# Optimization experiments

Measured on AMD Instinct MI355X. Metric: run time of the kernel, lower is better.

Reference implementation:

```python
import jax, jax.numpy as jnp
import numpy as np

H = 12          # num_heads
LENS_T = 64     # template tokens
LENS_S = 256    # search tokens
KEEP = int(0.7 * LENS_S)  # 179 kept search tokens


def _ln(x, s, b):
    mu = jnp.mean(x, axis=-1, keepdims=True)
    var = jnp.mean(jnp.square(x - mu), axis=-1, keepdims=True)
    return (x - mu) / jnp.sqrt(var + 1e-5) * s + b


def setup_inputs() -> dict:
    key = jax.random.key(0)
    ks = jax.random.split(key, 8)
    B, C, Hh = 32, 768, 3072
    N = LENS_T + LENS_S
    w = lambda k, shape: jax.random.normal(k, shape, jnp.float32) * 0.02
    return {
        "x": jax.random.normal(ks[0], (B, N, C), jnp.float32),
        "global_index_t": jnp.tile(jnp.arange(LENS_T, dtype=jnp.int32), (B, 1)),
        "global_index_s": jnp.tile(jnp.arange(LENS_S, dtype=jnp.int32), (B, 1)),
        "norm1_s": jnp.ones((C,), jnp.float32), "norm1_b": jnp.zeros((C,), jnp.float32),
        "qkv_w": w(ks[1], (C, 3 * C)), "qkv_b": jnp.zeros((3 * C,), jnp.float32),
        "proj_w": w(ks[2], (C, C)), "proj_b": jnp.zeros((C,), jnp.float32),
        "norm2_s": jnp.ones((C,), jnp.float32), "norm2_b": jnp.zeros((C,), jnp.float32),
        "fc1_w": w(ks[3], (C, Hh)), "fc1_b": jnp.zeros((Hh,), jnp.float32),
        "fc2_w": w(ks[4], (Hh, C)), "fc2_b": jnp.zeros((C,), jnp.float32),
        "gcn_w": w(ks[5], (C, C)), "gcn_b": jnp.zeros((C,), jnp.float32),
        "norm3_s": jnp.ones((C,), jnp.float32), "norm3_b": jnp.zeros((C,), jnp.float32),
    }


def reference(x, global_index_t, global_index_s,
              norm1_s, norm1_b, qkv_w, qkv_b, proj_w, proj_b,
              norm2_s, norm2_b, fc1_w, fc1_b, fc2_w, fc2_b,
              gcn_w, gcn_b, norm3_s, norm3_b):
    B, N, C = x.shape
    hd = C // H
    scale = hd ** -0.5

    # --- attention (attn weights explicitly materialized) ---
    h = _ln(x, norm1_s, norm1_b)
    qkv = (h @ qkv_w + qkv_b).reshape(B, N, 3, H, hd).transpose(2, 0, 3, 1, 4)
    q, k, v = qkv[0], qkv[1], qkv[2]                      # [B,H,N,hd]
    attn = jax.nn.softmax(jnp.einsum('bhqd,bhkd->bhqk', q, k) * scale, axis=-1)
    xa = jnp.einsum('bhqk,bhkd->bhqd', attn, v).transpose(0, 2, 1, 3).reshape(B, N, C)
    xa = xa @ proj_w + proj_b
    x = x + xa

    # --- MLP ---
    x_res = x
    h2 = _ln(x, norm2_s, norm2_b)
    h2 = jax.nn.gelu(h2 @ fc1_w + fc1_b, approximate=False) @ fc2_w + fc2_b
    x = x_res + h2

    # --- GCN using template<->search attention as adjacency ---
    # adjacency = [[0, w_ts], [w_ts^T, 0]]; exploit block sparsity instead of
    # materializing the dense [B,N,N] matrix.
    w_ts = jnp.sum(attn[:, :, :LENS_T, LENS_T:], axis=1) / H   # [B,T,S]
    w_ts = jax.nn.softmax(w_ts, axis=2)
    support = x @ gcn_w + gcn_b
    out_t = jnp.einsum('bts,bsd->btd', w_ts, support[:, LENS_T:])   # top block
    out_s = jnp.einsum('bts,btd->bsd', w_ts, support[:, :LENS_T])   # bottom block
    x = jnp.concatenate([out_t, out_s], axis=1)
    x = x + _ln(x, norm3_s, norm3_b)

    # --- top-k token pruning on search tokens ---
    score_s = jnp.mean(attn[:, :, :LENS_T, LENS_T:], axis=(1, 2))   # [B,S]
    order = jnp.argsort(-score_s, axis=1)
    keep_indices = order[:, :KEEP]
    removed_index_s = order[:, KEEP:]
    gs_new = jnp.take_along_axis(global_index_s, keep_indices, axis=1)
    idx = jnp.concatenate([global_index_t.astype(jnp.int32), keep_indices + LENS_T], axis=1)
    x = jnp.take_along_axis(x, jnp.broadcast_to(idx[..., None], (B, idx.shape[1], C)), axis=1)
    return (x, global_index_t, gs_new, removed_index_s, attn)
```

## Files before the change

kernel.cpp:

```cpp
#include <hip/hip_runtime.h>
#include <math.h>

#define NKEEP 179
#define NREM  77
#define NOUT_ROWS 243

typedef __bf16 bf16x8 __attribute__((ext_vector_type(8)));
typedef float f32x4 __attribute__((ext_vector_type(4)));

__device__ __forceinline__ unsigned short f2bf(float f) {
  unsigned u = __builtin_bit_cast(unsigned, f);
  u = (u + 0x7FFFu + ((u >> 16) & 1u)) >> 16;
  return (unsigned short)u;
}

__device__ __forceinline__ void gload_lds16(const void* g, void* l) {
  __builtin_amdgcn_global_load_lds((const __attribute__((address_space(1))) void*)g,
                                   (__attribute__((address_space(3))) void*)l,
                                   16, 0, 0);
}

template<int RESID, int OUTMODE>
__global__ __launch_bounds__(256)
void ln_kernel(const float* __restrict__ in, const float* __restrict__ gs,
               const float* __restrict__ gb, void* __restrict__ outp,
               void* __restrict__ outp2) {
  int row = blockIdx.x;
  const float* p = in + (size_t)row * 768;
  int tid = threadIdx.x;
  float v0 = p[tid], v1 = p[tid + 256], v2 = p[tid + 512];
  __shared__ double rs[256], rq[256];
  double d0 = v0, d1 = v1, d2 = v2;
  rs[tid] = d0 + d1 + d2;
  rq[tid] = d0 * d0 + d1 * d1 + d2 * d2;
  __syncthreads();
  for (int st = 128; st > 0; st >>= 1) {
    if (tid < st) { rs[tid] += rs[tid + st]; rq[tid] += rq[tid + st]; }
    __syncthreads();
  }
  double mu  = rs[0] * (1.0 / 768.0);
  double var = rq[0] * (1.0 / 768.0) - mu * mu;
  float rstd = (float)rsqrt(var + 1e-5);
  float muf = (float)mu;
  float y0 = (v0 - muf) * rstd * gs[tid]       + gb[tid];
  float y1 = (v1 - muf) * rstd * gs[tid + 256] + gb[tid + 256];
  float y2 = (v2 - muf) * rstd * gs[tid + 512] + gb[tid + 512];
  if (RESID) { y0 += v0; y1 += v1; y2 += v2; }
  if (OUTMODE == 0 || OUTMODE == 2) {
    float* o = (float*)outp + (size_t)row * 768;
    o[tid] = y0; o[tid + 256] = y1; o[tid + 512] = y2;
  }
  if (OUTMODE == 1) {
    unsigned short* o = (unsigned short*)outp + (size_t)row * 768;
    o[tid] = f2bf(y0); o[tid + 256] = f2bf(y1); o[tid + 512] = f2bf(y2);
  }
  if (OUTMODE == 2) {
    unsigned short* o = (unsigned short*)outp2 + (size_t)row * 768;
    o[tid] = f2bf(y0); o[tid + 256] = f2bf(y1); o[tid + 512] = f2bf(y2);
  }
}

__global__ __launch_bounds__(256)
void wtrans_kernel(const float* __restrict__ W, unsigned short* __restrict__ Wt,
                   int K, int N) {
  __shared__ float t[32][33];
  int n0 = blockIdx.x * 32, k0 = blockIdx.y * 32;
  int tid = threadIdx.x;
#pragma unroll
  for (int p = 0; p < 4; p++) {
    int idx = tid + p * 256;
    int r = idx >> 5, c = idx & 31;
    t[r][c] = W[(size_t)(k0 + r) * N + n0 + c];
  }
  __syncthreads();
#pragma unroll
  for (int p = 0; p < 4; p++) {
    int idx = tid + p * 256;
    int r = idx >> 5, c = idx & 31;
    Wt[(size_t)(n0 + r) * K + k0 + c] = f2bf(t[c][r]);
  }
}

template<int ACT, int RES, int OUTBF>
__global__ __launch_bounds__(256)
void gemm_bf16_kernel(const unsigned short* __restrict__ A,
                      const unsigned short* __restrict__ Bt,
                      const float* __restrict__ bias, const float* __restrict__ res,
                      void* __restrict__ outp, int M, int K, int N) {
  __shared__ unsigned short Al[128 * 64];
  __shared__ unsigned short Bl[128 * 64];
  int tid = threadIdx.x;
  int lane = tid & 63, wid = tid >> 6;
  int wr = wid >> 1, wc = wid & 1;
  int bm0 = blockIdx.y * 128, bn0 = blockIdx.x * 128;

  int r8 = lane >> 3;
  int csw = lane & 7;
  int csrc = csw ^ r8;

  const unsigned short* Abase = A + (size_t)bm0 * K + (size_t)csrc * 8;
  const unsigned short* Bbase = Bt + (size_t)bn0 * K + (size_t)csrc * 8;

  f32x4 acc[4][4] = {};

  int mrow = lane & 15;
  int kch = lane >> 4;
  int key = mrow & 7;

  for (int k0 = 0; k0 < K; k0 += 64) {
#pragma unroll
    for (int i = 0; i < 4; i++) {
      int rr = wid * 32 + i * 8;
      gload_lds16(Abase + (size_t)(rr + r8) * K + k0, Al + rr * 64);
      gload_lds16(Bbase + (size_t)(rr + r8) * K + k0, Bl + rr * 64);
    }
    __syncthreads();
#pragma unroll
    for (int ks = 0; ks < 2; ks++) {
      bf16x8 af[4], bfr[4];
#pragma unroll
      for (int f = 0; f < 4; f++) {
        int ra = wr * 64 + f * 16 + mrow;
        int ca = (ks * 4 + kch) ^ key;
        af[f] = *reinterpret_cast<const bf16x8*>(&Al[ra * 64 + ca * 8]);
        int rb = wc * 64 + f * 16 + mrow;
        bfr[f] = *reinterpret_cast<const bf16x8*>(&Bl[rb * 64 + ca * 8]);
      }
#pragma unroll
      for (int fm = 0; fm < 4; fm++)
#pragma unroll
        for (int fn = 0; fn < 4; fn++)
          acc[fm][fn] = __builtin_amdgcn_mfma_f32_16x16x32_bf16(
              af[fm], bfr[fn], acc[fm][fn], 0, 0, 0);
    }
    __syncthreads();
  }
#pragma unroll
  for (int fm = 0; fm < 4; fm++) {
#pragma unroll
    for (int j = 0; j < 4; j++) {
      int row = bm0 + wr * 64 + fm * 16 + (lane >> 4) * 4 + j;
#pragma unroll
      for (int fn = 0; fn < 4; fn++) {
        int col = bn0 + wc * 64 + fn * 16 + (lane & 15);
        float c = acc[fm][fn][j] + bias[col];
        if (ACT == 1) c = 0.5f * c * (1.0f + erff(c * 0.70710678118654752f));
        if (RES) c += res[(size_t)row * N + col];
        if (OUTBF) ((unsigned short*)outp)[(size_t)row * N + col] = f2bf(c);
        else       ((float*)outp)[(size_t)row * N + col] = c;
      }
    }
  }
}

__global__ __launch_bounds__(256)
void gemm_qkv_bf16_kernel(const unsigned short* __restrict__ A,
                          const unsigned short* __restrict__ Bt,
                          const float* __restrict__ bias,
                          float* __restrict__ Qb, float* __restrict__ Vb) {
  __shared__ unsigned short Al[128 * 64];
  __shared__ unsigned short Bl[128 * 64];
  const int K = 768;
  int tid = threadIdx.x;
  int lane = tid & 63, wid = tid >> 6;
  int wr = wid >> 1, wc = wid & 1;
  int bx = blockIdx.x;
  int colbase = (bx < 6) ? bx * 128 : (bx - 6) * 128 + 1536;
  int bm0 = blockIdx.y * 128;

  int r8 = lane >> 3;
  int csw = lane & 7;
  int csrc = csw ^ r8;

  const unsigned short* Abase = A + (size_t)bm0 * K + (size_t)csrc * 8;
  const unsigned short* Bbase = Bt + (size_t)colbase * K + (size_t)csrc * 8;

  f32x4 acc[4][4] = {};
  int mrow = lane & 15;
  int kch = lane >> 4;
  int key = mrow & 7;

  for (int k0 = 0; k0 < K; k0 += 64) {
#pragma unroll
    for (int i = 0; i < 4; i++) {
      int rr = wid * 32 + i * 8;
      gload_lds16(Abase + (size_t)(rr + r8) * K + k0, Al + rr * 64);
      gload_lds16(Bbase + (size_t)(rr + r8) * K + k0, Bl + rr * 64);
    }
    __syncthreads();
#pragma unroll
    for (int ks = 0; ks < 2; ks++) {
      bf16x8 af[4], bfr[4];
#pragma unroll
      for (int f = 0; f < 4; f++) {
        int ra = wr * 64 + f * 16 + mrow;
        int ca = (ks * 4 + kch) ^ key;
        af[f] = *reinterpret_cast<const bf16x8*>(&Al[ra * 64 + ca * 8]);
        int rb = wc * 64 + f * 16 + mrow;
        bfr[f] = *reinterpret_cast<const bf16x8*>(&Bl[rb * 64 + ca * 8]);
      }
#pragma unroll
      for (int fm = 0; fm < 4; fm++)
#pragma unroll
        for (int fn = 0; fn < 4; fn++)
          acc[fm][fn] = __builtin_amdgcn_mfma_f32_16x16x32_bf16(
              af[fm], bfr[fn], acc[fm][fn], 0, 0, 0);
    }
    __syncthreads();
  }
#pragma unroll
  for (int fm = 0; fm < 4; fm++) {
#pragma unroll
    for (int j = 0; j < 4; j++) {
      int row = bm0 + wr * 64 + fm * 16 + (lane >> 4) * 4 + j;
      int b = row / 320, nr = row - b * 320;
#pragma unroll
      for (int fn = 0; fn < 4; fn++) {
        int col = colbase + wc * 64 + fn * 16 + (lane & 15);
        int sel = col / 768;
        int rem = col - sel * 768;
        int h = rem >> 6, d = rem & 63;
        float* dstb = (sel == 0) ? Qb : Vb;
        dstb[(((size_t)(b * 12 + h) * 320 + nr) << 6) + d] = acc[fm][fn][j] + bias[col];
      }
    }
  }
}

template<int ROWMAP>
__global__ __launch_bounds__(256)
void gemm_prec_kernel(const float* __restrict__ A, const float* __restrict__ W,
                      const float* __restrict__ bias, int colOff,
                      float* __restrict__ Dst) {
  __shared__ float As[64][20];
  __shared__ float Bs[16][64];
  int tid = threadIdx.x;
  int tx = tid & 15, ty = tid >> 4;
  int bm0 = blockIdx.y * 64, bn0 = blockIdx.x * 64;
  int sm = tid >> 2, sc4 = tid & 3;
  int br = tid >> 4, bc4 = tid & 15;
  int arow;
  if (ROWMAP) { int m = bm0 + sm; arow = (m >> 6) * 320 + (m & 63); }
  else        { arow = bm0 + sm; }
  const float* Aptr = A + (size_t)arow * 768 + sc4 * 4;
  const float* Wptr = W + (size_t)br * 2304 + colOff + bn0 + bc4 * 4;

  double master[4][4] = {};
  for (int k0 = 0; k0 < 768; k0 += 16) {
    float4 av = *(const float4*)(Aptr + k0);
    float4 bv = *(const float4*)(Wptr + (size_t)k0 * 2304);
    __syncthreads();
    *(float4*)&As[sm][sc4 * 4] = av;
    *(float4*)&Bs[br][bc4 * 4] = bv;
    __syncthreads();
    float chunk[4][4] = {};
#pragma unroll
    for (int kk = 0; kk < 16; kk++) {
      float a[4], bb[4];
      *(float4*)bb = *(const float4*)&Bs[kk][tx * 4];
#pragma unroll
      for (int i = 0; i < 4; i++) a[i] = As[ty * 4 + i][kk];
#pragma unroll
      for (int i = 0; i < 4; i++)
#pragma unroll
        for (int j = 0; j < 4; j++) chunk[i][j] = fmaf(a[i], bb[j], chunk[i][j]);
    }
#pragma unroll
    for (int i = 0; i < 4; i++)
#pragma unroll
      for (int j = 0; j < 4; j++) master[i][j] += (double)chunk[i][j];
  }
  int n0 = bn0 + tx * 4;
  int h = n0 >> 6, d = n0 & 63;
#pragma unroll
  for (int i = 0; i < 4; i++) {
    int m = bm0 + ty * 4 + i;
    int b, nr;
    if (ROWMAP) { b = m >> 6; nr = m & 63; }
    else        { b = m / 320; nr = m - b * 320; }
    float* dst = Dst + (((size_t)(b * 12 + h) * 320 + nr) << 6) + d;
    float4 v;
    v.x = (float)master[i][0] + bias[colOff + n0];
    v.y = (float)master[i][1] + bias[colOff + n0 + 1];
    v.z = (float)master[i][2] + bias[colOff + n0 + 2];
    v.w = (float)master[i][3] + bias[colOff + n0 + 3];
    *(float4*)dst = v;
  }
}

__global__ __launch_bounds__(256)
void attn_fused_kernel(const float* __restrict__ Qb, const float* __restrict__ Kb,
                       const float* __restrict__ Vb, float* __restrict__ attn,
                       unsigned short* __restrict__ xa) {
  __shared__ float Qs[64][68];
  __shared__ float Ks[64][68];
  int qt = blockIdx.x, h = blockIdx.y, b = blockIdx.z;
  int bh = b * 12 + h;
  int q0 = qt * 64;
  int t = threadIdx.x;
  int tx = t & 15, ty = t >> 4;
  const float* Qg = Qb + (((size_t)bh * 320 + q0) << 6);
  const float* Kg = Kb + (((size_t)bh * 320) << 6);
  const float* Vg = Vb + (((size_t)bh * 320) << 6);
  float* attn_bh = attn + ((size_t)bh * 320 + q0) * 320;

  {
    int r = t >> 2, c = (t & 3) * 16;
    const float* src = Qg + (r << 6) + c;
#pragma unroll
    for (int i = 0; i < 4; i++)
      *(float4*)&Qs[r][c + i * 4] = *(const float4*)(src + i * 4);
  }

  float s[4][20];
  float mrow[4] = {-1e30f, -1e30f, -1e30f, -1e30f};

#pragma unroll
  for (int kc = 0; kc < 5; ++kc) {
    __syncthreads();
    {
      int r = t >> 2, c = (t & 3) * 16;
      const float* src = Kg + ((size_t)(kc * 64 + r) << 6) + c;
#pragma unroll
      for (int i = 0; i < 4; i++)
        *(float4*)&Ks[r][c + i * 4] = *(const float4*)(src + i * 4);
    }
    __syncthreads();
    float acc[4][4] = {};
#pragma unroll 4
    for (int d0 = 0; d0 < 64; d0 += 4) {
      float4 qv[4], kv[4];
#pragma unroll
      for (int i = 0; i < 4; i++) qv[i] = *(const float4*)&Qs[ty * 4 + i][d0];
#pragma unroll
      for (int j = 0; j < 4; j++) kv[j] = *(const float4*)&Ks[tx * 4 + j][d0];
#pragma unroll
      for (int i = 0; i < 4; i++)
#pragma unroll
        for (int j = 0; j < 4; j++) {
          acc[i][j] = fmaf(qv[i].x, kv[j].x, acc[i][j]);
          acc[i][j] = fmaf(qv[i].y, kv[j].y, acc[i][j]);
          acc[i][j] = fmaf(qv[i].z, kv[j].z, acc[i][j]);
          acc[i][j] = fmaf(qv[i].w, kv[j].w, acc[i][j]);
        }
    }
#pragma unroll
    for (int i = 0; i < 4; i++) {
      float sx = acc[i][0] * 0.125f, sy = acc[i][1] * 0.125f;
      float sz = acc[i][2] * 0.125f, sw = acc[i][3] * 0.125f;
      mrow[i] = fmaxf(mrow[i], fmaxf(fmaxf(sx, sy), fmaxf(sz, sw)));
      s[i][kc * 4 + 0] = sx; s[i][kc * 4 + 1] = sy;
      s[i][kc * 4 + 2] = sz; s[i][kc * 4 + 3] = sw;
    }
  }
#pragma unroll
  for (int i = 0; i < 4; i++) {
    mrow[i] = fmaxf(mrow[i], __shfl_xor(mrow[i], 1, 16));
    mrow[i] = fmaxf(mrow[i], __shfl_xor(mrow[i], 2, 16));
    mrow[i] = fmaxf(mrow[i], __shfl_xor(mrow[i], 4, 16));
    mrow[i] = fmaxf(mrow[i], __shfl_xor(mrow[i], 8, 16));
  }

  double lsum[4] = {0.0, 0.0, 0.0, 0.0};
#pragma unroll
  for (int i = 0; i < 4; i++)
#pragma unroll
    for (int c = 0; c < 20; c++) {
      float e = expf(s[i][c] - mrow[i]);
      s[i][c] = e;
      lsum[i] += (double)e;
    }
#pragma unroll
  for (int i = 0; i < 4; i++) {
    lsum[i] += __shfl_xor(lsum[i], 1, 16);
    lsum[i] += __shfl_xor(lsum[i], 2, 16);
    lsum[i] += __shfl_xor(lsum[i], 4, 16);
    lsum[i] += __shfl_xor(lsum[i], 8, 16);
  }
  float inv[4];
#pragma unroll
  for (int i = 0; i < 4; i++) inv[i] = (float)(1.0 / lsum[i]);

#pragma unroll
  for (int i = 0; i < 4; i++)
#pragma unroll
    for (int kc = 0; kc < 5; kc++) {
      float4 sv;
      sv.x = s[i][kc * 4 + 0] * inv[i];
      sv.y = s[i][kc * 4 + 1] * inv[i];
      sv.z = s[i][kc * 4 + 2] * inv[i];
      sv.w = s[i][kc * 4 + 3] * inv[i];
      *(float4*)&attn_bh[(size_t)(ty * 4 + i) * 320 + kc * 64 + tx * 4] = sv;
    }
  __syncthreads();

  float acc2[4][4] = {};
  for (int kc = 0; kc < 5; ++kc) {
    __syncthreads();
    {
      int r = t >> 2, c = (t & 3) * 16;
      const float* src = Vg + ((size_t)(kc * 64 + r) << 6) + c;
#pragma unroll
      for (int i = 0; i < 4; i++)
        *(float4*)&Ks[r][c + i * 4] = *(const float4*)(src + i * 4);
    }
    __syncthreads();
#pragma unroll 4
    for (int kk4 = 0; kk4 < 16; ++kk4) {
      int k = kc * 64 + kk4 * 4;
      float4 pv[4], vv[4];
#pragma unroll
      for (int i = 0; i < 4; i++)
        pv[i] = *(const float4*)&attn_bh[(size_t)(ty * 4 + i) * 320 + k];
#pragma unroll
      for (int l = 0; l < 4; l++) vv[l] = *(const float4*)&Ks[kk4 * 4 + l][tx * 4];
#pragma unroll
      for (int i = 0; i < 4; i++) {
        acc2[i][0] = fmaf(pv[i].x, vv[0].x, acc2[i][0]);
        acc2[i][1] = fmaf(pv[i].x, vv[0].y, acc2[i][1]);
        acc2[i][2] = fmaf(pv[i].x, vv[0].z, acc2[i][2]);
        acc2[i][3] = fmaf(pv[i].x, vv[0].w, acc2[i][3]);
        acc2[i][0] = fmaf(pv[i].y, vv[1].x, acc2[i][0]);
        acc2[i][1] = fmaf(pv[i].y, vv[1].y, acc2[i][1]);
        acc2[i][2] = fmaf(pv[i].y, vv[1].z, acc2[i][2]);
        acc2[i][3] = fmaf(pv[i].y, vv[1].w, acc2[i][3]);
        acc2[i][0] = fmaf(pv[i].z, vv[2].x, acc2[i][0]);
        acc2[i][1] = fmaf(pv[i].z, vv[2].y, acc2[i][1]);
        acc2[i][2] = fmaf(pv[i].z, vv[2].z, acc2[i][2]);
        acc2[i][3] = fmaf(pv[i].z, vv[2].w, acc2[i][3]);
        acc2[i][0] = fmaf(pv[i].w, vv[3].x, acc2[i][0]);
        acc2[i][1] = fmaf(pv[i].w, vv[3].y, acc2[i][1]);
        acc2[i][2] = fmaf(pv[i].w, vv[3].z, acc2[i][2]);
        acc2[i][3] = fmaf(pv[i].w, vv[3].w, acc2[i][3]);
      }
    }
  }
#pragma unroll
  for (int i = 0; i < 4; i++) {
    unsigned short* dst = xa + (size_t)(b * 320 + q0 + ty * 4 + i) * 768 + h * 64 + tx * 4;
    uint2 pk;
    pk.x = (unsigned)f2bf(acc2[i][0]) | ((unsigned)f2bf(acc2[i][1]) << 16);
    pk.y = (unsigned)f2bf(acc2[i][2]) | ((unsigned)f2bf(acc2[i][3]) << 16);
    *(uint2*)dst = pk;
  }
}

__global__ __launch_bounds__(256)
void wts_kernel(const float* __restrict__ attn, float* __restrict__ wts) {
  int bid = blockIdx.x;
  int tt = bid & 63, b = bid >> 6;
  int s = threadIdx.x;
  float acc = 0.0f;
  const float* base = attn + (((size_t)(b * 12)) * 320 + tt) * 320 + 64 + s;
#pragma unroll
  for (int h = 0; h < 12; h++) acc += base[(size_t)h * 320 * 320];
  acc *= (1.0f / 12.0f);
  __shared__ float red[256];
  red[s] = acc; __syncthreads();
  for (int st = 128; st > 0; st >>= 1) {
    if (s < st) red[s] = fmaxf(red[s], red[s + st]);
    __syncthreads();
  }
  float m = red[0]; __syncthreads();
  float e = expf(acc - m);
  red[s] = e; __syncthreads();
  for (int st = 128; st > 0; st >>= 1) {
    if (s < st) red[s] += red[s + st];
    __syncthreads();
  }
  wts[(size_t)bid * 256 + s] = e / red[0];
}

__global__ __launch_bounds__(256)
void out_t_kernel(const float* __restrict__ wts, const float* __restrict__ sup,
                  float* __restrict__ x3) {
  int idx = blockIdx.x * 256 + threadIdx.x;
  int c = idx % 768;
  int tt = (idx / 768) % 64;
  int b = idx / (768 * 64);
  const float* wrow = wts + (size_t)(b * 64 + tt) * 256;
  const float* sp = sup + ((size_t)(b * 320 + 64)) * 768 + c;
  float acc = 0.0f;
  for (int s = 0; s < 256; s++) acc = fmaf(wrow[s], sp[(size_t)s * 768], acc);
  x3[((size_t)(b * 320 + tt)) * 768 + c] = acc;
}

__global__ __launch_bounds__(256)
void out_s_kernel(const float* __restrict__ wts, const float* __restrict__ sup,
                  float* __restrict__ x3) {
  int idx = blockIdx.x * 256 + threadIdx.x;
  int c = idx % 768;
  int s = (idx / 768) % 256;
  int b = idx / (768 * 256);
  const float* wp = wts + (size_t)(b * 64) * 256 + s;
  const float* sp = sup + ((size_t)(b * 320)) * 768 + c;
  float acc = 0.0f;
#pragma unroll 4
  for (int tt = 0; tt < 64; tt++) acc = fmaf(wp[(size_t)tt * 256], sp[(size_t)tt * 768], acc);
  x3[((size_t)(b * 320 + 64 + s)) * 768 + c] = acc;
}

__global__ __launch_bounds__(256)
void score_part_kernel(const float* __restrict__ attn, double* __restrict__ part) {
  int h = blockIdx.x, b = blockIdx.y;
  int s = threadIdx.x;
  const float* base = attn + (((size_t)(b * 12 + h)) * 320) * 320 + 64 + s;
  double acc = 0.0;
  for (int tt = 0; tt < 64; tt++) acc += (double)base[(size_t)tt * 320];
  part[((size_t)(b * 12 + h)) * 256 + s] = acc;
}

__global__ __launch_bounds__(256)
void score_final_kernel(const double* __restrict__ part, const int* __restrict__ git,
                        const int* __restrict__ gis, int* __restrict__ order_ws,
                        float* __restrict__ out_git, float* __restrict__ out_gs,
                        float* __restrict__ out_rm) {
  int b = blockIdx.x, s = threadIdx.x;
  double acc = 0.0;
#pragma unroll
  for (int h = 0; h < 12; h++) acc += part[((size_t)(b * 12 + h)) * 256 + s];
  __shared__ double sc[256];
  __shared__ int ord[256];
  sc[s] = acc;
  __syncthreads();
  double my = sc[s];
  int r = 0;
  for (int i = 0; i < 256; i++) {
    double si = sc[i];
    r += (si > my) || (si == my && i < s);
  }
  ord[r] = s;
  __syncthreads();
  int o = ord[s];
  order_ws[b * 256 + s] = o;
  if (s < NKEEP) out_gs[b * NKEEP + s] = (float)gis[b * 256 + o];
  else           out_rm[b * NREM + (s - NKEEP)] = (float)o;
  if (s < 64)    out_git[b * 64 + s] = (float)git[b * 64 + s];
}

__global__ __launch_bounds__(256)
void gather_kernel(const float* __restrict__ x3, const int* __restrict__ git,
                   const int* __restrict__ order_ws, float* __restrict__ out) {
  int bid = blockIdx.x;
  int j = bid % NOUT_ROWS, b = bid / NOUT_ROWS;
  int src = (j < 64) ? git[b * 64 + j] : (order_ws[b * 256 + (j - 64)] + 64);
  const float* p = x3 + ((size_t)(b * 320 + src)) * 768;
  float* o = out + ((size_t)(b * NOUT_ROWS + j)) * 768;
  int tid = threadIdx.x;
  o[tid] = p[tid]; o[tid + 256] = p[tid + 256]; o[tid + 512] = p[tid + 512];
}

extern "C" void kernel_launch(void* const* d_in, const int* in_sizes, int n_in,
                              void* d_out, int out_size, void* d_ws, size_t ws_size,
                              hipStream_t stream) {
  (void)in_sizes; (void)n_in; (void)out_size; (void)ws_size;
  const float* x      = (const float*)d_in[0];
  const int*   git    = (const int*)d_in[1];
  const int*   gis    = (const int*)d_in[2];
  const float* n1s    = (const float*)d_in[3];
  const float* n1b    = (const float*)d_in[4];
  const float* qkv_w  = (const float*)d_in[5];
  const float* qkv_b  = (const float*)d_in[6];
  const float* proj_w = (const float*)d_in[7];
  const float* proj_b = (const float*)d_in[8];
  const float* n2s    = (const float*)d_in[9];
  const float* n2b    = (const float*)d_in[10];
  const float* fc1_w  = (const float*)d_in[11];
  const float* fc1_b  = (const float*)d_in[12];
  const float* fc2_w  = (const float*)d_in[13];
  const float* fc2_b  = (const float*)d_in[14];
  const float* gcn_w  = (const float*)d_in[15];
  const float* gcn_b  = (const float*)d_in[16];
  const float* n3s    = (const float*)d_in[17];
  const float* n3b    = (const float*)d_in[18];

  float* out     = (float*)d_out;
  float* out_x   = out;
  float* out_git = out + 5971968;
  float* out_gs  = out + 5974016;
  float* out_rm  = out + 5979744;
  float* attn    = out + 5982208;

  float* w      = (float*)d_ws;
  float* bufA   = w;
  float* bufB   = w + 7864320;
  float* bufBIG = w + 15728640;
  float* Qbuf = bufBIG;
  float* Kbuf = bufBIG + 7864320;
  float* Vbuf = bufBIG + 15728640;
  unsigned short* ln1_bf = (unsigned short*)(bufBIG + 23592960);
  unsigned short* f1_bf = (unsigned short*)bufBIG;
  unsigned short* x2_bf = (unsigned short*)(bufBIG + 15728640);
  float* x3 = bufBIG + 19660800;
  unsigned short* wbf = (unsigned short*)(bufBIG + 27525120);
  unsigned short* proj_wt = wbf;
  unsigned short* fc1_wt  = wbf + 589824;
  unsigned short* fc2_wt  = fc1_wt + 2359296;
  unsigned short* gcn_wt  = fc2_wt + 2359296;
  unsigned short* qkv_wt  = gcn_wt + 589824;
  unsigned short* xa_bf = (unsigned short*)bufA;
  unsigned short* h2_bf = (unsigned short*)bufA;
  float* wts    = bufBIG + 31457280;
  int*   order_ws = (int*)(wts + 524288);
  double* partd  = (double*)(wts + 524288 + 8192);

  const int M = 10240;

  wtrans_kernel<<<dim3(24, 24), dim3(256), 0, stream>>>(proj_w, proj_wt, 768, 768);
  wtrans_kernel<<<dim3(96, 24), dim3(256), 0, stream>>>(fc1_w, fc1_wt, 768, 3072);
  wtrans_kernel<<<dim3(24, 96), dim3(256), 0, stream>>>(fc2_w, fc2_wt, 3072, 768);
  wtrans_kernel<<<dim3(24, 24), dim3(256), 0, stream>>>(gcn_w, gcn_wt, 768, 768);
  wtrans_kernel<<<dim3(72, 24), dim3(256), 0, stream>>>(qkv_w, qkv_wt, 768, 2304);

  ln_kernel<0, 2><<<dim3(M), dim3(256), 0, stream>>>(x, n1s, n1b, bufA, ln1_bf);
  gemm_qkv_bf16_kernel<<<dim3(12, 80), dim3(256), 0, stream>>>(
      ln1_bf, qkv_wt, qkv_b, Qbuf, Vbuf);
  gemm_prec_kernel<0><<<dim3(12, 160), dim3(256), 0, stream>>>(
      bufA, qkv_w, qkv_b, 768, Kbuf);
  gemm_prec_kernel<1><<<dim3(12, 32), dim3(256), 0, stream>>>(
      bufA, qkv_w, qkv_b, 0, Qbuf);
  attn_fused_kernel<<<dim3(5, 12, 32), dim3(256), 0, stream>>>(
      Qbuf, Kbuf, Vbuf, attn, xa_bf);
  gemm_bf16_kernel<0, 1, 0><<<dim3(768 / 128, M / 128), dim3(256), 0, stream>>>(
      xa_bf, proj_wt, proj_b, x, bufB, M, 768, 768);
  ln_kernel<0, 1><<<dim3(M), dim3(256), 0, stream>>>(bufB, n2s, n2b, h2_bf, nullptr);
  gemm_bf16_kernel<1, 0, 1><<<dim3(3072 / 128, M / 128), dim3(256), 0, stream>>>(
      h2_bf, fc1_wt, fc1_b, nullptr, f1_bf, M, 768, 3072);
  gemm_bf16_kernel<0, 1, 1><<<dim3(768 / 128, M / 128), dim3(256), 0, stream>>>(
      f1_bf, fc2_wt, fc2_b, bufB, x2_bf, M, 3072, 768);
  wts_kernel<<<dim3(32 * 64), dim3(256), 0, stream>>>(attn, wts);
  gemm_bf16_kernel<0, 0, 0><<<dim3(768 / 128, M / 128), dim3(256), 0, stream>>>(
      x2_bf, gcn_wt, gcn_b, nullptr, bufA, M, 768, 768);
  out_t_kernel<<<dim3(32 * 64 * 768 / 256), dim3(256), 0, stream>>>(wts, bufA, x3);
  out_s_kernel<<<dim3(32 * 256 * 768 / 256), dim3(256), 0, stream>>>(wts, bufA, x3);
  ln_kernel<1, 0><<<dim3(M), dim3(256), 0, stream>>>(x3, n3s, n3b, x3, nullptr);
  score_part_kernel<<<dim3(12, 32), dim3(256), 0, stream>>>(attn, partd);
  score_final_kernel<<<dim3(32), dim3(256), 0, stream>>>(partd, git, gis, order_ws,
                                                         out_git, out_gs, out_rm);
  gather_kernel<<<dim3(32 * NOUT_ROWS), dim3(256), 0, stream>>>(x3, git,
                                                                order_ws, out_x);
}
```

Before: 1.058 ms.

## Swap GEMM grid order, retile fp32 precision GEMM, stage attention probs in LDS

All bf16 GEMM launches swap grid axes so consecutive blocks walk M while sharing the same weight column tile, aiming for better L2 reuse of weights. The high-precision fp32 K/Q GEMM now loads 32-wide K chunks, stores A transposed in LDS for float4 reads, and does half as many outer iterations. The attention kernel flattens its grid and stages normalized probabilities in shared memory instead of re-reading them from the global attn output during P·V. This trades an extra LDS write per chunk for removing the global re-read and one barrier.

```diff
diff --git a/kernel.cpp b/kernel.cpp
--- a/kernel.cpp
+++ b/kernel.cpp
@@ -92,7 +92,7 @@
   int tid = threadIdx.x;
   int lane = tid & 63, wid = tid >> 6;
   int wr = wid >> 1, wc = wid & 1;
-  int bm0 = blockIdx.y * 128, bn0 = blockIdx.x * 128;
+  int bm0 = blockIdx.x * 128, bn0 = blockIdx.y * 128;
 
   int r8 = lane >> 3;
   int csw = lane & 7;
@@ -164,9 +164,9 @@
   int tid = threadIdx.x;
   int lane = tid & 63, wid = tid >> 6;
   int wr = wid >> 1, wc = wid & 1;
-  int bx = blockIdx.x;
-  int colbase = (bx < 6) ? bx * 128 : (bx - 6) * 128 + 1536;
-  int bm0 = blockIdx.y * 128;
+  int by = blockIdx.y;
+  int colbase = (by < 6) ? by * 128 : (by - 6) * 128 + 1536;
+  int bm0 = blockIdx.x * 128;
 
   int r8 = lane >> 3;
   int csw = lane & 7;
@@ -232,43 +232,63 @@
 void gemm_prec_kernel(const float* __restrict__ A, const float* __restrict__ W,
                       const float* __restrict__ bias, int colOff,
                       float* __restrict__ Dst) {
-  __shared__ float As[64][20];
-  __shared__ float Bs[16][64];
+  __shared__ float AsT[32][68];
+  __shared__ float Bs[32][68];
   int tid = threadIdx.x;
   int tx = tid & 15, ty = tid >> 4;
-  int bm0 = blockIdx.y * 64, bn0 = blockIdx.x * 64;
-  int sm = tid >> 2, sc4 = tid & 3;
-  int br = tid >> 4, bc4 = tid & 15;
-  int arow;
-  if (ROWMAP) { int m = bm0 + sm; arow = (m >> 6) * 320 + (m & 63); }
-  else        { arow = bm0 + sm; }
-  const float* Aptr = A + (size_t)arow * 768 + sc4 * 4;
-  const float* Wptr = W + (size_t)br * 2304 + colOff + bn0 + bc4 * 4;
+  int bm0 = blockIdx.x * 64, bn0 = blockIdx.y * 64;
+
+  int arow[2];
+#pragma unroll
+  for (int q = 0; q < 2; q++) {
+    int idx = tid + q * 256;
+    int m = bm0 + (idx >> 3);
+    arow[q] = ROWMAP ? ((m >> 6) * 320 + (m & 63)) : m;
+  }
+  const float* Wbase = W + colOff + bn0;
 
   double master[4][4] = {};
-  for (int k0 = 0; k0 < 768; k0 += 16) {
-    float4 av = *(const float4*)(Aptr + k0);
-    float4 bv = *(const float4*)(Wptr + (size_t)k0 * 2304);
-    __syncthreads();
-    *(float4*)&As[sm][sc4 * 4] = av;
-    *(float4*)&Bs[br][bc4 * 4] = bv;
-    __syncthreads();
-    float chunk[4][4] = {};
-#pragma unroll
-    for (int kk = 0; kk < 16; kk++) {
-      float a[4], bb[4];
-      *(float4*)bb = *(const float4*)&Bs[kk][tx * 4];
-#pragma unroll
-      for (int i = 0; i < 4; i++) a[i] = As[ty * 4 + i][kk];
+  for (int k0 = 0; k0 < 768; k0 += 32) {
+    float4 av[2], bv[2];
+#pragma unroll
+    for (int q = 0; q < 2; q++) {
+      int idx = tid + q * 256;
+      av[q] = *(const float4*)(A + (size_t)arow[q] * 768 + k0 + (idx & 7) * 4);
+      int br = idx >> 4, bc4 = idx & 15;
+      bv[q] = *(const float4*)(Wbase + (size_t)(k0 + br) * 2304 + bc4 * 4);
+    }
+    __syncthreads();
+#pragma unroll
+    for (int q = 0; q < 2; q++) {
+      int idx = tid + q * 256;
+      int r = idx >> 3, kc8 = idx & 7;
+      AsT[kc8 * 4 + 0][r] = av[q].x;
+      AsT[kc8 * 4 + 1][r] = av[q].y;
+      AsT[kc8 * 4 + 2][r] = av[q].z;
+      AsT[kc8 * 4 + 3][r] = av[q].w;
+      *(float4*)&Bs[idx >> 4][(idx & 15) * 4] = bv[q];
+    }
+    __syncthreads();
+#pragma unroll
+    for (int half = 0; half < 2; half++) {
+      float chunk[4][4] = {};
+#pragma unroll
+      for (int kk = 0; kk < 16; kk++) {
+        int kkk = half * 16 + kk;
+        float a[4], bb[4];
+        *(float4*)a  = *(const float4*)&AsT[kkk][ty * 4];
+        *(float4*)bb = *(const float4*)&Bs[kkk][tx * 4];
+#pragma unroll
+        for (int i = 0; i < 4; i++)
+#pragma unroll
+          for (int j = 0; j < 4; j++) chunk[i][j] = fmaf(a[i], bb[j], chunk[i][j]);
+      }
 #pragma unroll
       for (int i = 0; i < 4; i++)
 #pragma unroll
-        for (int j = 0; j < 4; j++) chunk[i][j] = fmaf(a[i], bb[j], chunk[i][j]);
-    }
-#pragma unroll
-    for (int i = 0; i < 4; i++)
-#pragma unroll
-      for (int j = 0; j < 4; j++) master[i][j] += (double)chunk[i][j];
+        for (int j = 0; j < 4; j++) master[i][j] += (double)chunk[i][j];
+    }
+    __syncthreads();
   }
   int n0 = bn0 + tx * 4;
   int h = n0 >> 6, d = n0 & 63;
@@ -294,8 +314,10 @@
                        unsigned short* __restrict__ xa) {
   __shared__ float Qs[64][68];
   __shared__ float Ks[64][68];
-  int qt = blockIdx.x, h = blockIdx.y, b = blockIdx.z;
-  int bh = b * 12 + h;
+  float (*Ps)[68] = Qs;
+  int bid = blockIdx.x;
+  int qt = bid / 384, bh = bid % 384;
+  int h = bh % 12, b = bh / 12;
   int q0 = qt * 64;
   int t = threadIdx.x;
   int tx = t & 15, ty = t >> 4;
@@ -392,7 +414,6 @@
       sv.w = s[i][kc * 4 + 3] * inv[i];
       *(float4*)&attn_bh[(size_t)(ty * 4 + i) * 320 + kc * 64 + tx * 4] = sv;
     }
-  __syncthreads();
 
   float acc2[4][4] = {};
   for (int kc = 0; kc < 5; ++kc) {
@@ -404,14 +425,22 @@
       for (int i = 0; i < 4; i++)
         *(float4*)&Ks[r][c + i * 4] = *(const float4*)(src + i * 4);
     }
+#pragma unroll
+    for (int i = 0; i < 4; i++) {
+      float4 sv;
+      sv.x = s[i][kc * 4 + 0] * inv[i];
+      sv.y = s[i][kc * 4 + 1] * inv[i];
+      sv.z = s[i][kc * 4 + 2] * inv[i];
+      sv.w = s[i][kc * 4 + 3] * inv[i];
+      *(float4*)&Ps[ty * 4 + i][tx * 4] = sv;
+    }
     __syncthreads();
 #pragma unroll 4
     for (int kk4 = 0; kk4 < 16; ++kk4) {
-      int k = kc * 64 + kk4 * 4;
       float4 pv[4], vv[4];
 #pragma unroll
       for (int i = 0; i < 4; i++)
-        pv[i] = *(const float4*)&attn_bh[(size_t)(ty * 4 + i) * 320 + k];
+        pv[i] = *(const float4*)&Ps[ty * 4 + i][kk4 * 4];
 #pragma unroll
       for (int l = 0; l < 4; l++) vv[l] = *(const float4*)&Ks[kk4 * 4 + l][tx * 4];
 #pragma unroll
@@ -613,23 +642,23 @@
   wtrans_kernel<<<dim3(72, 24), dim3(256), 0, stream>>>(qkv_w, qkv_wt, 768, 2304);
 
   ln_kernel<0, 2><<<dim3(M), dim3(256), 0, stream>>>(x, n1s, n1b, bufA, ln1_bf);
-  gemm_qkv_bf16_kernel<<<dim3(12, 80), dim3(256), 0, stream>>>(
+  gemm_qkv_bf16_kernel<<<dim3(80, 12), dim3(256), 0, stream>>>(
       ln1_bf, qkv_wt, qkv_b, Qbuf, Vbuf);
-  gemm_prec_kernel<0><<<dim3(12, 160), dim3(256), 0, stream>>>(
+  gemm_prec_kernel<0><<<dim3(160, 12), dim3(256), 0, stream>>>(
       bufA, qkv_w, qkv_b, 768, Kbuf);
-  gemm_prec_kernel<1><<<dim3(12, 32), dim3(256), 0, stream>>>(
+  gemm_prec_kernel<1><<<dim3(32, 12), dim3(256), 0, stream>>>(
       bufA, qkv_w, qkv_b, 0, Qbuf);
-  attn_fused_kernel<<<dim3(5, 12, 32), dim3(256), 0, stream>>>(
+  attn_fused_kernel<<<dim3(1920), dim3(256), 0, stream>>>(
       Qbuf, Kbuf, Vbuf, attn, xa_bf);
-  gemm_bf16_kernel<0, 1, 0><<<dim3(768 / 128, M / 128), dim3(256), 0, stream>>>(
+  gemm_bf16_kernel<0, 1, 0><<<dim3(M / 128, 768 / 128), dim3(256), 0, stream>>>(
       xa_bf, proj_wt, proj_b, x, bufB, M, 768, 768);
   ln_kernel<0, 1><<<dim3(M), dim3(256), 0, stream>>>(bufB, n2s, n2b, h2_bf, nullptr);
-  gemm_bf16_kernel<1, 0, 1><<<dim3(3072 / 128, M / 128), dim3(256), 0, stream>>>(
+  gemm_bf16_kernel<1, 0, 1><<<dim3(M / 128, 3072 / 128), dim3(256), 0, stream>>>(
       h2_bf, fc1_wt, fc1_b, nullptr, f1_bf, M, 768, 3072);
-  gemm_bf16_kernel<0, 1, 1><<<dim3(768 / 128, M / 128), dim3(256), 0, stream>>>(
+  gemm_bf16_kernel<0, 1, 1><<<dim3(M / 128, 768 / 128), dim3(256), 0, stream>>>(
       f1_bf, fc2_wt, fc2_b, bufB, x2_bf, M, 3072, 768);
   wts_kernel<<<dim3(32 * 64), dim3(256), 0, stream>>>(attn, wts);
-  gemm_bf16_kernel<0, 0, 0><<<dim3(768 / 128, M / 128), dim3(256), 0, stream>>>(
+  gemm_bf16_kernel<0, 0, 0><<<dim3(M / 128, 768 / 128), dim3(256), 0, stream>>>(
       x2_bf, gcn_wt, gcn_b, nullptr, bufA, M, 768, 768);
   out_t_kernel<<<dim3(32 * 64 * 768 / 256), dim3(256), 0, stream>>>(wts, bufA, x3);
   out_s_kernel<<<dim3(32 * 256 * 768 / 256), dim3(256), 0, stream>>>(wts, bufA, x3);
```

Result: faster. 1.015 ms (-4.1%).
